# Optimization experiments

Hardware: AMD Instinct MI355X
Metric: run time of the kernel (lower is better)

Reference implementation:

```python
import jax, jax.numpy as jnp
import numpy as np

B, L, V, D = 8, 2048, 1024, 512  # batch, seq (max_len), vocab_size (input feat), embedding_dim

def setup_inputs() -> dict:
    key = jax.random.key(0)
    kx, kq, kk, kv = jax.random.split(key, 4)
    scale = 1.0 / np.sqrt(V)
    return {
        "x": jax.random.normal(kx, (B, L, V), dtype=jnp.float32),
        "Wq": jax.random.uniform(kq, (D, V), dtype=jnp.float32, minval=-scale, maxval=scale),
        "Wk": jax.random.uniform(kk, (D, V), dtype=jnp.float32, minval=-scale, maxval=scale),
        "Wv": jax.random.uniform(kv, (D, V), dtype=jnp.float32, minval=-scale, maxval=scale),
    }

def reference(x, Wq, Wk, Wv):
    # nn.Linear without bias: y = x @ W.T
    q = jnp.einsum('blv,dv->bld', x, Wq)
    k = jnp.einsum('blv,dv->bld', x, Wk)
    v = jnp.einsum('blv,dv->bld', x, Wv)
    scores = jnp.einsum('bqd,bkd->bqk', q, k) / jnp.sqrt(jnp.float32(D))
    attn = jax.nn.softmax(scores, axis=2)
    return jnp.einsum('bqk,bkd->bqd', attn, v)
```

## Files before the change

### kernel.cpp

```cpp
#include <hip/hip_runtime.h>
#include <cstdint>
#include <cstddef>


typedef __attribute__((ext_vector_type(8))) __bf16 bf16x8;
typedef __attribute__((ext_vector_type(4))) float f32x4;
typedef __attribute__((ext_vector_type(16))) float f32x16;
typedef __attribute__((ext_vector_type(4))) unsigned short ushort4v;

__device__ __forceinline__ unsigned short f2bf(float f) {
  unsigned u = __float_as_uint(f);
  return (unsigned short)((u + 0x7fffu + ((u >> 16) & 1u)) >> 16);
}

__device__ __forceinline__ void async_load16(const unsigned short* g, unsigned short* l) {
  __builtin_amdgcn_global_load_lds(
      (__attribute__((address_space(1))) void*)(g),
      (__attribute__((address_space(3))) void*)(l), 16, 0, 0);
}

__global__ __launch_bounds__(256) void cvt_f32_bf16(const float* __restrict__ src,
                                                    unsigned short* __restrict__ dst) {
  int i = (blockIdx.x * 256 + threadIdx.x) * 4;
  float4 v = *(const float4*)(src + i);
  ushort4v o;
  o.x = f2bf(v.x); o.y = f2bf(v.y); o.z = f2bf(v.z); o.w = f2bf(v.w);
  *(ushort4v*)(dst + i) = o;
}

__global__ __launch_bounds__(256) void cvt_w3(const float* __restrict__ a,
                                              const float* __restrict__ b,
                                              const float* __restrict__ c,
                                              unsigned short* __restrict__ dst,
                                              float* __restrict__ rowsum) {
  int bx = blockIdx.x;
  if (bx < 16) {
    int j = (bx * 256 + threadIdx.x) * 4;
    *(float4*)(rowsum + j) = make_float4(0.f, 0.f, 0.f, 0.f);
  }
  const float* src = (bx < 512) ? a : (bx < 1024) ? b : c;
  int seg = (bx < 512) ? 0 : (bx < 1024) ? 1 : 2;
  int i = ((bx & 511) * 256 + threadIdx.x) * 4;
  float4 v = *(const float4*)(src + i);
  ushort4v o;
  o.x = f2bf(v.x); o.y = f2bf(v.y); o.z = f2bf(v.z); o.w = f2bf(v.w);
  *(ushort4v*)(dst + seg * 524288 + i) = o;
}

__global__ __launch_bounds__(256) void gemm_qkv(
    const unsigned short* __restrict__ A,
    const unsigned short* __restrict__ Bw,
    unsigned short* __restrict__ qk,
    unsigned short* __restrict__ vT) {
  __shared__ unsigned short sA[128 * 64];
  __shared__ unsigned short sB[128 * 64];
  const int tid = threadIdx.x;
  const int lane = tid & 63, wid = tid >> 6;
  const int wm = wid & 1, wn = wid >> 1;
  const int l31 = lane & 31, half = lane >> 5;

  A += (size_t)blockIdx.y * 128 * 1024;
  Bw += (size_t)blockIdx.x * 128 * 1024;

  f32x16 acc[2][2] = {};

  for (int k0 = 0; k0 < 1024; k0 += 64) {
    __syncthreads();
    #pragma unroll
    for (int p = 0; p < 4; ++p) {
      int u = p * 256 + tid;
      int r = u >> 3, cs = (u & 7) ^ (r & 7);
      async_load16(&A[(size_t)r * 1024 + k0 + cs * 8], &sA[u * 8]);
      async_load16(&Bw[(size_t)r * 1024 + k0 + cs * 8], &sB[u * 8]);
    }
    __syncthreads();

    #pragma unroll
    for (int ks = 0; ks < 4; ++ks) {
      int cb = ks * 2 + half;
      bf16x8 aF[2], bF[2];
      #pragma unroll
      for (int i = 0; i < 2; ++i) {
        int rA = wm * 64 + i * 32 + l31;
        aF[i] = *(const bf16x8*)&sA[(rA * 8 + (cb ^ (rA & 7))) * 8];
        int rB = wn * 64 + i * 32 + l31;
        bF[i] = *(const bf16x8*)&sB[(rB * 8 + (cb ^ (rB & 7))) * 8];
      }
      #pragma unroll
      for (int mt = 0; mt < 2; ++mt)
        #pragma unroll
        for (int nt = 0; nt < 2; ++nt)
          acc[mt][nt] = __builtin_amdgcn_mfma_f32_32x32x16_bf16(
              aF[mt], bF[nt], acc[mt][nt], 0, 0, 0);
    }
  }

  if (blockIdx.x < 8) {
    unsigned short* Cc = qk + (size_t)blockIdx.y * 128 * 1024 + (size_t)blockIdx.x * 128;
    #pragma unroll
    for (int mt = 0; mt < 2; ++mt)
      #pragma unroll
      for (int nt = 0; nt < 2; ++nt) {
        int col = wn * 64 + nt * 32 + l31;
        #pragma unroll
        for (int q = 0; q < 4; ++q) {
          int row = wm * 64 + mt * 32 + half * 4 + q * 8;
          #pragma unroll
          for (int r2 = 0; r2 < 4; ++r2)
            Cc[(size_t)(row + r2) * 1024 + col] = f2bf(acc[mt][nt][q * 4 + r2]);
        }
      }
  } else {
    int nvx = blockIdx.x - 8;
    #pragma unroll
    for (int mt = 0; mt < 2; ++mt)
      #pragma unroll
      for (int nt = 0; nt < 2; ++nt) {
        int d = nvx * 128 + wn * 64 + nt * 32 + l31;
        #pragma unroll
        for (int q = 0; q < 4; ++q) {
          int grow = blockIdx.y * 128 + wm * 64 + mt * 32 + half * 4 + q * 8;
          int b = grow >> 11, l = grow & 2047;
          ushort4v o;
          o.x = f2bf(acc[mt][nt][q * 4 + 0]); o.y = f2bf(acc[mt][nt][q * 4 + 1]);
          o.z = f2bf(acc[mt][nt][q * 4 + 2]); o.w = f2bf(acc[mt][nt][q * 4 + 3]);
          *(ushort4v*)&vT[(size_t)b * 1048576 + (size_t)d * 2048 + l] = o;
        }
      }
  }
}

__global__ __launch_bounds__(256) void gemm_exp(
    const unsigned short* __restrict__ qk,
    unsigned short* __restrict__ S, float scale,
    float* __restrict__ rowsum) {
  __shared__ unsigned short sA[128 * 64];
  __shared__ unsigned short sB[128 * 64];
  const int tid = threadIdx.x;
  const int lane = tid & 63, wid = tid >> 6;
  const int wm = wid & 1, wn = wid >> 1;
  const int l15 = lane & 15, lq = lane >> 4;

  const unsigned short* A = qk + (size_t)blockIdx.z * 2097152 + (size_t)blockIdx.y * 128 * 1024;
  const unsigned short* Bk = qk + 512 + (size_t)blockIdx.z * 2097152 + (size_t)blockIdx.x * 128 * 1024;

  f32x4 acc[4][4] = {};

  for (int k0 = 0; k0 < 512; k0 += 64) {
    __syncthreads();
    #pragma unroll
    for (int p = 0; p < 4; ++p) {
      int u = p * 256 + tid;
      int r = u >> 3, cs = (u & 7) ^ (r & 7);
      async_load16(&A[(size_t)r * 1024 + k0 + cs * 8], &sA[u * 8]);
      async_load16(&Bk[(size_t)r * 1024 + k0 + cs * 8], &sB[u * 8]);
    }
    __syncthreads();

    #pragma unroll
    for (int kk = 0; kk < 2; ++kk) {
      bf16x8 aF[4], bF[4];
      int cb = kk * 4 + lq;
      #pragma unroll
      for (int i = 0; i < 4; ++i) {
        int rA = wm * 64 + i * 16 + l15;
        aF[i] = *(const bf16x8*)&sA[(rA * 8 + (cb ^ (rA & 7))) * 8];
        int rB = wn * 64 + i * 16 + l15;
        bF[i] = *(const bf16x8*)&sB[(rB * 8 + (cb ^ (rB & 7))) * 8];
      }
      #pragma unroll
      for (int mt = 0; mt < 4; ++mt)
        #pragma unroll
        for (int nt = 0; nt < 4; ++nt)
          acc[mt][nt] = __builtin_amdgcn_mfma_f32_16x16x32_bf16(
              aF[mt], bF[nt], acc[mt][nt], 0, 0, 0);
    }
  }

  unsigned short* Cc = S + (size_t)blockIdx.z * 4194304 +
                       (size_t)blockIdx.y * 128 * 2048 + (size_t)blockIdx.x * 128;
  #pragma unroll
  for (int mt = 0; mt < 4; ++mt) {
    float rs0 = 0.f, rs1 = 0.f, rs2 = 0.f, rs3 = 0.f;
    #pragma unroll
    for (int nt = 0; nt < 4; ++nt) {
      #pragma unroll
      for (int r2 = 0; r2 < 4; ++r2)
        acc[mt][nt][r2] = __expf(acc[mt][nt][r2] * scale);
      rs0 += acc[mt][nt][0]; rs1 += acc[mt][nt][1];
      rs2 += acc[mt][nt][2]; rs3 += acc[mt][nt][3];
    }
    #pragma unroll
    for (int off = 1; off < 16; off <<= 1) {
      rs0 += __shfl_xor(rs0, off, 64); rs1 += __shfl_xor(rs1, off, 64);
      rs2 += __shfl_xor(rs2, off, 64); rs3 += __shfl_xor(rs3, off, 64);
    }
    if (l15 == 0) {
      int gr = blockIdx.z * 2048 + blockIdx.y * 128 + wm * 64 + mt * 16 + lq * 4;
      atomicAdd(&rowsum[gr], rs0); atomicAdd(&rowsum[gr + 1], rs1);
      atomicAdd(&rowsum[gr + 2], rs2); atomicAdd(&rowsum[gr + 3], rs3);
    }
    #pragma unroll
    for (int nt = 0; nt < 4; ++nt) {
      int row = wm * 64 + mt * 16 + lq * 4;
      int col = wn * 64 + nt * 16 + l15;
      #pragma unroll
      for (int r2 = 0; r2 < 4; ++r2)
        Cc[(size_t)(row + r2) * 2048 + col] = f2bf(acc[mt][nt][r2]);
    }
  }
}

__global__ __launch_bounds__(256) void gemm_pv(
    const unsigned short* __restrict__ P, const unsigned short* __restrict__ vT,
    const float* __restrict__ rowsum, float* __restrict__ out) {
  __shared__ unsigned short sA[128 * 64];
  __shared__ unsigned short sB[128 * 64];
  const int tid = threadIdx.x;
  const int lane = tid & 63, wid = tid >> 6;
  const int wm = wid & 1, wn = wid >> 1;
  const int l31 = lane & 31, half = lane >> 5;
  const int b = blockIdx.z;
  const int m0 = blockIdx.y * 128, n0 = blockIdx.x * 128;
  const unsigned short* A = P + (size_t)b * 4194304 + (size_t)m0 * 2048;
  const unsigned short* Bv = vT + (size_t)b * 1048576 + (size_t)n0 * 2048;

  f32x16 acc[2][2] = {};

  for (int k0 = 0; k0 < 2048; k0 += 64) {
    __syncthreads();
    #pragma unroll
    for (int p = 0; p < 4; ++p) {
      int u = p * 256 + tid;
      int r = u >> 3, cs = (u & 7) ^ (r & 7);
      async_load16(&A[(size_t)r * 2048 + k0 + cs * 8], &sA[u * 8]);
      async_load16(&Bv[(size_t)r * 2048 + k0 + cs * 8], &sB[u * 8]);
    }
    __syncthreads();

    #pragma unroll
    for (int ks = 0; ks < 4; ++ks) {
      int cb = ks * 2 + half;
      bf16x8 aF[2], bF[2];
      #pragma unroll
      for (int i = 0; i < 2; ++i) {
        int rA = wm * 64 + i * 32 + l31;
        aF[i] = *(const bf16x8*)&sA[(rA * 8 + (cb ^ (rA & 7))) * 8];
        int rB = wn * 64 + i * 32 + l31;
        bF[i] = *(const bf16x8*)&sB[(rB * 8 + (cb ^ (rB & 7))) * 8];
      }
      #pragma unroll
      for (int mt = 0; mt < 2; ++mt)
        #pragma unroll
        for (int nt = 0; nt < 2; ++nt)
          acc[mt][nt] = __builtin_amdgcn_mfma_f32_32x32x16_bf16(
              aF[mt], bF[nt], acc[mt][nt], 0, 0, 0);
    }
  }

  #pragma unroll
  for (int mt = 0; mt < 2; ++mt) {
    #pragma unroll
    for (int q = 0; q < 4; ++q) {
      int row = m0 + wm * 64 + mt * 32 + half * 4 + q * 8;
      float4 rs = *(const float4*)&rowsum[(size_t)b * 2048 + row];
      float inv0 = __builtin_amdgcn_rcpf(rs.x), inv1 = __builtin_amdgcn_rcpf(rs.y);
      float inv2 = __builtin_amdgcn_rcpf(rs.z), inv3 = __builtin_amdgcn_rcpf(rs.w);
      #pragma unroll
      for (int nt = 0; nt < 2; ++nt) {
        int col = n0 + wn * 64 + nt * 32 + l31;
        float* op = out + ((size_t)b * 2048 + row) * 512 + col;
        op[0]    = acc[mt][nt][q * 4 + 0] * inv0;
        op[512]  = acc[mt][nt][q * 4 + 1] * inv1;
        op[1024] = acc[mt][nt][q * 4 + 2] * inv2;
        op[1536] = acc[mt][nt][q * 4 + 3] * inv3;
      }
    }
  }
}

extern "C" void kernel_launch(void* const* d_in, const int* in_sizes, int n_in,
                              void* d_out, int out_size, void* d_ws, size_t ws_size,
                              hipStream_t stream) {
  const float* x  = (const float*)d_in[0];
  const float* Wq = (const float*)d_in[1];
  const float* Wk = (const float*)d_in[2];
  const float* Wv = (const float*)d_in[3];
  float* out = (float*)d_out;
  char* ws = (char*)d_ws;

  unsigned short* xb = (unsigned short*)ws;
  unsigned short* S  = (unsigned short*)ws;
  unsigned short* wf = (unsigned short*)(ws + 33554432);
  unsigned short* qk = (unsigned short*)(ws + 67108864);
  unsigned short* vT = (unsigned short*)(ws + 100663296);
  float* rowsum = (float*)(ws + 117440512);

  const float rsqrtD = 0.044194173824159216f;

  hipLaunchKernelGGL(cvt_f32_bf16, dim3(16384), dim3(256), 0, stream, x, xb);
  hipLaunchKernelGGL(cvt_w3, dim3(1536), dim3(256), 0, stream, Wq, Wk, Wv, wf, rowsum);

  hipLaunchKernelGGL(gemm_qkv, dim3(12, 128, 1), dim3(256), 0, stream, xb, wf, qk, vT);

  hipLaunchKernelGGL(gemm_exp, dim3(16, 16, 8), dim3(256), 0, stream,
                     qk, S, rsqrtD, rowsum);

  hipLaunchKernelGGL(gemm_pv, dim3(4, 16, 8), dim3(256), 0, stream, S, vT, rowsum, out);

  (void)in_sizes; (void)n_in; (void)out_size; (void)ws_size;
}
```

Measured before the change: 292.6 us.

## Compute softmax row sums in PV GEMM from bf16 P instead of atomics

```diff
diff --git a/kernel.cpp b/kernel.cpp
--- a/kernel.cpp
+++ b/kernel.cpp
@@ -4,9 +4,9 @@
 
 
 typedef __attribute__((ext_vector_type(8))) __bf16 bf16x8;
-typedef __attribute__((ext_vector_type(4))) float f32x4;
 typedef __attribute__((ext_vector_type(16))) float f32x16;
 typedef __attribute__((ext_vector_type(4))) unsigned short ushort4v;
+typedef __attribute__((ext_vector_type(4))) unsigned int uint4v;
 
 __device__ __forceinline__ unsigned short f2bf(float f) {
   unsigned u = __float_as_uint(f);
@@ -31,13 +31,8 @@
 __global__ __launch_bounds__(256) void cvt_w3(const float* __restrict__ a,
                                               const float* __restrict__ b,
                                               const float* __restrict__ c,
-                                              unsigned short* __restrict__ dst,
-                                              float* __restrict__ rowsum) {
+                                              unsigned short* __restrict__ dst) {
   int bx = blockIdx.x;
-  if (bx < 16) {
-    int j = (bx * 256 + threadIdx.x) * 4;
-    *(float4*)(rowsum + j) = make_float4(0.f, 0.f, 0.f, 0.f);
-  }
   const float* src = (bx < 512) ? a : (bx < 1024) ? b : c;
   int seg = (bx < 512) ? 0 : (bx < 1024) ? 1 : 2;
   int i = ((bx & 511) * 256 + threadIdx.x) * 4;
@@ -132,19 +127,18 @@
 
 __global__ __launch_bounds__(256) void gemm_exp(
     const unsigned short* __restrict__ qk,
-    unsigned short* __restrict__ S, float scale,
-    float* __restrict__ rowsum) {
+    unsigned short* __restrict__ S, float scale) {
   __shared__ unsigned short sA[128 * 64];
   __shared__ unsigned short sB[128 * 64];
   const int tid = threadIdx.x;
   const int lane = tid & 63, wid = tid >> 6;
   const int wm = wid & 1, wn = wid >> 1;
-  const int l15 = lane & 15, lq = lane >> 4;
-
-  const unsigned short* A = qk + (size_t)blockIdx.z * 2097152 + (size_t)blockIdx.y * 128 * 1024;
+  const int l31 = lane & 31, half = lane >> 5;
+
+  const unsigned short* A  = qk + (size_t)blockIdx.z * 2097152 + (size_t)blockIdx.y * 128 * 1024;
   const unsigned short* Bk = qk + 512 + (size_t)blockIdx.z * 2097152 + (size_t)blockIdx.x * 128 * 1024;
 
-  f32x4 acc[4][4] = {};
+  f32x16 acc[2][2] = {};
 
   for (int k0 = 0; k0 < 512; k0 += 64) {
     __syncthreads();
@@ -158,21 +152,21 @@
     __syncthreads();
 
     #pragma unroll
-    for (int kk = 0; kk < 2; ++kk) {
-      bf16x8 aF[4], bF[4];
-      int cb = kk * 4 + lq;
-      #pragma unroll
-      for (int i = 0; i < 4; ++i) {
-        int rA = wm * 64 + i * 16 + l15;
+    for (int ks = 0; ks < 4; ++ks) {
+      int cb = ks * 2 + half;
+      bf16x8 aF[2], bF[2];
+      #pragma unroll
+      for (int i = 0; i < 2; ++i) {
+        int rA = wm * 64 + i * 32 + l31;
         aF[i] = *(const bf16x8*)&sA[(rA * 8 + (cb ^ (rA & 7))) * 8];
-        int rB = wn * 64 + i * 16 + l15;
+        int rB = wn * 64 + i * 32 + l31;
         bF[i] = *(const bf16x8*)&sB[(rB * 8 + (cb ^ (rB & 7))) * 8];
       }
       #pragma unroll
-      for (int mt = 0; mt < 4; ++mt)
-        #pragma unroll
-        for (int nt = 0; nt < 4; ++nt)
-          acc[mt][nt] = __builtin_amdgcn_mfma_f32_16x16x32_bf16(
+      for (int mt = 0; mt < 2; ++mt)
+        #pragma unroll
+        for (int nt = 0; nt < 2; ++nt)
+          acc[mt][nt] = __builtin_amdgcn_mfma_f32_32x32x16_bf16(
               aF[mt], bF[nt], acc[mt][nt], 0, 0, 0);
     }
   }
@@ -180,42 +174,27 @@
   unsigned short* Cc = S + (size_t)blockIdx.z * 4194304 +
                        (size_t)blockIdx.y * 128 * 2048 + (size_t)blockIdx.x * 128;
   #pragma unroll
-  for (int mt = 0; mt < 4; ++mt) {
-    float rs0 = 0.f, rs1 = 0.f, rs2 = 0.f, rs3 = 0.f;
-    #pragma unroll
-    for (int nt = 0; nt < 4; ++nt) {
-      #pragma unroll
-      for (int r2 = 0; r2 < 4; ++r2)
-        acc[mt][nt][r2] = __expf(acc[mt][nt][r2] * scale);
-      rs0 += acc[mt][nt][0]; rs1 += acc[mt][nt][1];
-      rs2 += acc[mt][nt][2]; rs3 += acc[mt][nt][3];
-    }
-    #pragma unroll
-    for (int off = 1; off < 16; off <<= 1) {
-      rs0 += __shfl_xor(rs0, off, 64); rs1 += __shfl_xor(rs1, off, 64);
-      rs2 += __shfl_xor(rs2, off, 64); rs3 += __shfl_xor(rs3, off, 64);
-    }
-    if (l15 == 0) {
-      int gr = blockIdx.z * 2048 + blockIdx.y * 128 + wm * 64 + mt * 16 + lq * 4;
-      atomicAdd(&rowsum[gr], rs0); atomicAdd(&rowsum[gr + 1], rs1);
-      atomicAdd(&rowsum[gr + 2], rs2); atomicAdd(&rowsum[gr + 3], rs3);
-    }
-    #pragma unroll
-    for (int nt = 0; nt < 4; ++nt) {
-      int row = wm * 64 + mt * 16 + lq * 4;
-      int col = wn * 64 + nt * 16 + l15;
-      #pragma unroll
-      for (int r2 = 0; r2 < 4; ++r2)
-        Cc[(size_t)(row + r2) * 2048 + col] = f2bf(acc[mt][nt][r2]);
-    }
-  }
+  for (int mt = 0; mt < 2; ++mt)
+    #pragma unroll
+    for (int nt = 0; nt < 2; ++nt) {
+      int col = wn * 64 + nt * 32 + l31;
+      #pragma unroll
+      for (int q = 0; q < 4; ++q) {
+        int row = wm * 64 + mt * 32 + half * 4 + q * 8;
+        #pragma unroll
+        for (int r2 = 0; r2 < 4; ++r2)
+          Cc[(size_t)(row + r2) * 2048 + col] =
+              f2bf(__expf(acc[mt][nt][q * 4 + r2] * scale));
+      }
+    }
 }
 
 __global__ __launch_bounds__(256) void gemm_pv(
     const unsigned short* __restrict__ P, const unsigned short* __restrict__ vT,
-    const float* __restrict__ rowsum, float* __restrict__ out) {
+    float* __restrict__ out) {
   __shared__ unsigned short sA[128 * 64];
   __shared__ unsigned short sB[128 * 64];
+  __shared__ float rs[128];
   const int tid = threadIdx.x;
   const int lane = tid & 63, wid = tid >> 6;
   const int wm = wid & 1, wn = wid >> 1;
@@ -226,6 +205,7 @@
   const unsigned short* Bv = vT + (size_t)b * 1048576 + (size_t)n0 * 2048;
 
   f32x16 acc[2][2] = {};
+  float rsum[2] = {0.f, 0.f};
 
   for (int k0 = 0; k0 < 2048; k0 += 64) {
     __syncthreads();
@@ -250,6 +230,14 @@
         bF[i] = *(const bf16x8*)&sB[(rB * 8 + (cb ^ (rB & 7))) * 8];
       }
       #pragma unroll
+      for (int i = 0; i < 2; ++i) {
+        uint4v u = __builtin_bit_cast(uint4v, aF[i]);
+        #pragma unroll
+        for (int t = 0; t < 4; ++t)
+          rsum[i] += __uint_as_float(u[t] << 16) +
+                     __uint_as_float(u[t] & 0xffff0000u);
+      }
+      #pragma unroll
       for (int mt = 0; mt < 2; ++mt)
         #pragma unroll
         for (int nt = 0; nt < 2; ++nt)
@@ -259,13 +247,22 @@
   }
 
   #pragma unroll
+  for (int i = 0; i < 2; ++i) {
+    rsum[i] += __shfl_xor(rsum[i], 32, 64);
+    if (lane < 32) rs[wm * 64 + i * 32 + lane] = rsum[i];
+  }
+  __syncthreads();
+
+  #pragma unroll
   for (int mt = 0; mt < 2; ++mt) {
     #pragma unroll
     for (int q = 0; q < 4; ++q) {
-      int row = m0 + wm * 64 + mt * 32 + half * 4 + q * 8;
-      float4 rs = *(const float4*)&rowsum[(size_t)b * 2048 + row];
-      float inv0 = __builtin_amdgcn_rcpf(rs.x), inv1 = __builtin_amdgcn_rcpf(rs.y);
-      float inv2 = __builtin_amdgcn_rcpf(rs.z), inv3 = __builtin_amdgcn_rcpf(rs.w);
+      int rl = wm * 64 + mt * 32 + half * 4 + q * 8;
+      int row = m0 + rl;
+      float inv0 = __builtin_amdgcn_rcpf(rs[rl]);
+      float inv1 = __builtin_amdgcn_rcpf(rs[rl + 1]);
+      float inv2 = __builtin_amdgcn_rcpf(rs[rl + 2]);
+      float inv3 = __builtin_amdgcn_rcpf(rs[rl + 3]);
       #pragma unroll
       for (int nt = 0; nt < 2; ++nt) {
         int col = n0 + wn * 64 + nt * 32 + l31;
@@ -294,19 +291,17 @@
   unsigned short* wf = (unsigned short*)(ws + 33554432);
   unsigned short* qk = (unsigned short*)(ws + 67108864);
   unsigned short* vT = (unsigned short*)(ws + 100663296);
-  float* rowsum = (float*)(ws + 117440512);
 
   const float rsqrtD = 0.044194173824159216f;
 
   hipLaunchKernelGGL(cvt_f32_bf16, dim3(16384), dim3(256), 0, stream, x, xb);
-  hipLaunchKernelGGL(cvt_w3, dim3(1536), dim3(256), 0, stream, Wq, Wk, Wv, wf, rowsum);
+  hipLaunchKernelGGL(cvt_w3, dim3(1536), dim3(256), 0, stream, Wq, Wk, Wv, wf);
 
   hipLaunchKernelGGL(gemm_qkv, dim3(12, 128, 1), dim3(256), 0, stream, xb, wf, qk, vT);
 
-  hipLaunchKernelGGL(gemm_exp, dim3(16, 16, 8), dim3(256), 0, stream,
-                     qk, S, rsqrtD, rowsum);
-
-  hipLaunchKernelGGL(gemm_pv, dim3(4, 16, 8), dim3(256), 0, stream, S, vT, rowsum, out);
+  hipLaunchKernelGGL(gemm_exp, dim3(16, 16, 8), dim3(256), 0, stream, qk, S, rsqrtD);
+
+  hipLaunchKernelGGL(gemm_pv, dim3(4, 16, 8), dim3(256), 0, stream, S, vT, out);
 
   (void)in_sizes; (void)n_in; (void)out_size; (void)ws_size;
 }
```

Result: faster. 277.1 us (-5.3%).
